# Kernel optimization log

Measured on AMD Instinct MI355X. Metric: run time of the kernel, lower is better.

## Reference

```python
import jax, jax.numpy as jnp
import numpy as np

N, E, D, H, C = 50000, 800000, 256, 8, 32  # C = D // H
STEPS = 6
NEG = 0.2  # leaky_relu negative slope (PyG HEATConv default)
ETD, EAD = 10, 50  # edge_type_emb_dim, edge_attr_emb_dim


def setup_inputs() -> dict:
    key = jax.random.key(0)
    ks = jax.random.split(key, 20)
    def g(k, shape, scale=0.05):
        return jax.random.normal(k, shape, dtype=jnp.float32) * scale
    return {
        "x": jax.random.normal(ks[0], (N, D), dtype=jnp.float32),
        "edge_index": jax.random.randint(ks[1], (2, E), 0, N),
        "edge_attr": jax.random.normal(ks[2], (E,), dtype=jnp.float32),
        "node_type": jax.random.randint(ks[3], (N,), 0, 2),
        "link_type": jax.random.randint(ks[4], (E,), 0, 3),
        # HEATConv params (shared across all 6 steps)
        "Wh": g(ks[5], (2, D, C)),          # HeteroLinear weight per node type
        "bh": g(ks[6], (2, C)),             # HeteroLinear bias per node type
        "Et": g(ks[7], (3, ETD)),           # edge type embedding table
        "Wea": g(ks[8], (1, EAD)),          # edge attr embedding (Linear, no bias)
        "Watt": g(ks[9], (2 * C + ETD + EAD, H)),  # attention (Linear, no bias)
        "Wlin": g(ks[10], (C + EAD, C)),    # message lin (Linear, no bias)
        # per-step FFN + LayerNorm params
        "ffn_w1": g(ks[11], (STEPS, D, 4 * D)),
        "ffn_b1": g(ks[12], (STEPS, 4 * D)),
        "ffn_w2": g(ks[13], (STEPS, 4 * D, D)),
        "ffn_b2": g(ks[14], (STEPS, D)),
        "ln1_g": jnp.ones((STEPS, D), jnp.float32),
        "ln1_b": jnp.zeros((STEPS, D), jnp.float32),
        "ln2_g": jnp.ones((STEPS, D), jnp.float32),
        "ln2_b": jnp.zeros((STEPS, D), jnp.float32),
    }


def _leaky(v):
    return jax.nn.leaky_relu(v, NEG)


def _layer_norm(h, g, b, eps=1e-5):
    mu = h.mean(-1, keepdims=True)
    var = h.var(-1, keepdims=True)  # biased, matches torch LayerNorm
    return (h - mu) * jax.lax.rsqrt(var + eps) * g + b


def _heat_conv(m, src, dst, edge_attr, node_type, link_type, Wh, bh, Et, Wea, Watt, Wlin):
    # node-type-specific linear (HeteroLinear, 2 types): compute both, select
    x_all = jnp.einsum('nd,tdc->tnc', m, Wh) + bh[:, None, :]     # [2,N,C]
    x = jnp.where(node_type[:, None] == 0, x_all[0], x_all[1])    # [N,C]
    ete = _leaky(Et[link_type])                                   # [E,ETD]
    eae = _leaky(edge_attr[:, None] @ Wea)                        # [E,EAD]
    feat = jnp.concatenate([x[dst], x[src], ete, eae], axis=-1)   # [E, 2C+ETD+EAD]
    logits = _leaky(feat @ Watt)                                  # [E,H]
    # segment softmax over incoming edges of each destination node
    mx = jax.ops.segment_max(logits, dst, num_segments=N)
    e = jnp.exp(logits - mx[dst])
    s = jax.ops.segment_sum(e, dst, num_segments=N)
    alpha = e / (s[dst] + 1e-16)                                  # [E,H]
    msg = jnp.concatenate([x[src], eae], axis=-1) @ Wlin          # [E,C]
    per_edge = alpha[:, :, None] * msg[:, None, :]                # [E,H,C]
    out = jax.ops.segment_sum(per_edge, dst, num_segments=N)      # [N,H,C]
    return out.reshape(N, H * C)  # concat heads; root_weight=False


def reference(x, edge_index, edge_attr, node_type, link_type, Wh, bh, Et, Wea, Watt, Wlin,
              ffn_w1, ffn_b1, ffn_w2, ffn_b2, ln1_g, ln1_b, ln2_g, ln2_b):
    src, dst = edge_index[0], edge_index[1]
    m = x
    for i in range(STEPS):
        h = _heat_conv(m, src, dst, edge_attr, node_type, link_type,
                       Wh, bh, Et, Wea, Watt, Wlin)
        m = _layer_norm(h + m, ln1_g[i], ln1_b[i])
        f = jax.nn.relu(m @ ffn_w1[i] + ffn_b1[i]) @ ffn_w2[i] + ffn_b2[i]
        m = _layer_norm(f + m, ln2_g[i], ln2_b[i])
    return m
```

## Files before the change

kernel.cpp:

```cpp
#include <hip/hip_runtime.h>

#define Nn 50000
#define Ee 800000
#define STEPSn 6
#define NP 49

typedef _Float16 half8 __attribute__((ext_vector_type(8)));
typedef _Float16 half4v __attribute__((ext_vector_type(4)));
typedef float floatx4 __attribute__((ext_vector_type(4)));

typedef __attribute__((address_space(1))) void gvoid_t;
typedef __attribute__((address_space(3))) void svoid_t;

__device__ __forceinline__ float leakyf(float v) { return v > 0.f ? v : 0.2f * v; }

__device__ __forceinline__ void gload16(const void* g, void* l) {
    __builtin_amdgcn_global_load_lds((const gvoid_t*)g, (svoid_t*)l, 16, 0, 0);
}

__global__ void k_count(const int* __restrict__ dst, int* __restrict__ cnt) {
    int e = blockIdx.x * 256 + threadIdx.x;
    if (e < Ee) atomicAdd(&cnt[dst[e]], 1);
}

__global__ __launch_bounds__(256) void k_scan1(const int* __restrict__ cnt,
                                               int* __restrict__ part) {
    int b = blockIdx.x, t = threadIdx.x;
    int s = 0;
#pragma unroll
    for (int j = 0; j < 4; ++j) {
        int idx = b * 1024 + j * 256 + t;
        if (idx < Nn) s += cnt[idx];
    }
#pragma unroll
    for (int d = 1; d < 64; d <<= 1) s += __shfl_xor(s, d);
    __shared__ int ws[4];
    if ((t & 63) == 0) ws[t >> 6] = s;
    __syncthreads();
    if (t == 0) part[b] = ws[0] + ws[1] + ws[2] + ws[3];
}

__global__ void k_scan2(const int* __restrict__ part, int* __restrict__ pref,
                        int* __restrict__ offN) {
    int t = threadIdx.x;
    int v = (t < NP) ? part[t] : 0;
    int p = v;
#pragma unroll
    for (int d = 1; d < 64; d <<= 1) {
        int u = __shfl_up(p, d);
        if (t >= d) p += u;
    }
    if (t < NP) pref[t] = p - v;
    if (t == 63) offN[0] = p;
}

__global__ __launch_bounds__(256) void k_scan3(const int* __restrict__ cnt,
                                               const int* __restrict__ pref,
                                               int* __restrict__ off) {
    __shared__ int wsum[4];
    int b = blockIdx.x, t = threadIdx.x;
    int base = b * 1024;
    int v[4];
    int s = 0;
#pragma unroll
    for (int j = 0; j < 4; ++j) {
        int idx = base + t * 4 + j;
        v[j] = (idx < Nn) ? cnt[idx] : 0;
        s += v[j];
    }
    int lane = t & 63, w = t >> 6;
    int ps = s;
#pragma unroll
    for (int d = 1; d < 64; d <<= 1) {
        int u = __shfl_up(ps, d);
        if (lane >= d) ps += u;
    }
    if (lane == 63) wsum[w] = ps;
    __syncthreads();
    int woff = 0;
    for (int i = 0; i < w; ++i) woff += wsum[i];
    int ex = pref[b] + woff + ps - s;
#pragma unroll
    for (int j = 0; j < 4; ++j) {
        int idx = base + t * 4 + j;
        if (idx < Nn) off[idx] = ex;
        ex += v[j];
    }
}

__global__ void k_fill(const int* __restrict__ src, const int* __restrict__ dst,
                       const float* __restrict__ edge_attr, const int* __restrict__ link_type,
                       const int* __restrict__ off, int* __restrict__ cur,
                       int2* __restrict__ edata) {
    int e = blockIdx.x * 256 + threadIdx.x;
    if (e >= Ee) return;
    int d = dst[e];
    int slot = off[d] + atomicAdd(&cur[d], 1);
    edata[slot] = make_int2(src[e] | (link_type[e] << 20), __float_as_int(edge_attr[e]));
}

__global__ void k_const(const float* __restrict__ Et, const float* __restrict__ Wea,
                        const float* __restrict__ Watt, const float* __restrict__ Wlin,
                        float* __restrict__ C) {
    __shared__ float u[50], v[50];
    int t = threadIdx.x;
    if (t < 50) {
        float w = Wea[t];
        u[t] = w * (w > 0.f ? 1.f : 0.2f);
        v[t] = w * (w < 0.f ? 1.f : 0.2f);
    }
    __syncthreads();
    if (t < 8) {
        float a = 0.f, b = 0.f;
        for (int j = 0; j < 50; ++j) {
            float w = Watt[(74 + j) * 8 + t];
            a += u[j] * w;
            b += v[j] * w;
        }
        C[t] = a;
        C[8 + t] = b;
    } else if (t < 32) {
        int lt = (t - 8) >> 3, h = (t - 8) & 7;
        float a = 0.f;
        for (int j = 0; j < 10; ++j) a += leakyf(Et[lt * 10 + j]) * Watt[(64 + j) * 8 + h];
        C[16 + (t - 8)] = a;
    } else if (t < 64) {
        int c = t - 32;
        float a = 0.f, b = 0.f;
        for (int j = 0; j < 50; ++j) {
            float w = Wlin[(32 + j) * 32 + c];
            a += u[j] * w;
            b += v[j] * w;
        }
        C[40 + c] = a;
        C[72 + c] = b;
    }
}

__global__ void k_comb(const float* __restrict__ Wh, const float* __restrict__ bh,
                       const float* __restrict__ Watt, const float* __restrict__ Wlin,
                       _Float16* __restrict__ Wcmb, float* __restrict__ bcmb) {
    int n = blockIdx.x;
    int k = threadIdx.x;
    if (n >= 96) {
        Wcmb[n * 256 + k] = (_Float16)0.f;
        return;
    }
    int ty = n / 48, c = n % 48;
    float a = 0.f;
    for (int kk = 0; kk < 32; ++kk) {
        float wsel;
        if (c < 32) wsel = Wlin[kk * 32 + c];
        else if (c < 40) wsel = Watt[kk * 8 + (c - 32)];
        else wsel = Watt[(32 + kk) * 8 + (c - 40)];
        a += Wh[ty * 8192 + k * 32 + kk] * wsel;
    }
    Wcmb[n * 256 + k] = (_Float16)a;
    if (k == 0) {
        float b = 0.f;
        for (int kk = 0; kk < 32; ++kk) {
            float wsel;
            if (c < 32) wsel = Wlin[kk * 32 + c];
            else if (c < 40) wsel = Watt[kk * 8 + (c - 32)];
            else wsel = Watt[(32 + kk) * 8 + (c - 40)];
            b += bh[ty * 32 + kk] * wsel;
        }
        bcmb[n] = b;
    }
}

__global__ void k_cvt(const float* __restrict__ x, _Float16* __restrict__ mh) {
    long i = ((long)blockIdx.x * 256 + threadIdx.x) * 4;
    if (i < (long)Nn * 256) {
        float4 v = *(const float4*)(x + i);
        half4v h;
        h[0] = (_Float16)v.x; h[1] = (_Float16)v.y;
        h[2] = (_Float16)v.z; h[3] = (_Float16)v.w;
        *(half4v*)(mh + i) = h;
    }
}

__global__ __launch_bounds__(256) void k_wtrans(const float* __restrict__ W,
                                                _Float16* __restrict__ WT,
                                                int K, int NN) {
    __shared__ float tile[64][65];
    int nk = K >> 6, nn = NN >> 6;
    int b = blockIdx.x;
    int s = b / (nk * nn);
    int r = b % (nk * nn);
    int kt = r / nn, nt = r % nn;
    const float* Ws = W + (long)s * K * NN;
    _Float16* WTs = WT + (long)s * K * NN;
    int lrow = threadIdx.x >> 6, lcol = threadIdx.x & 63;
#pragma unroll
    for (int i = 0; i < 16; ++i) {
        int row = i * 4 + lrow;
        tile[row][lcol] = Ws[(long)(kt * 64 + row) * NN + nt * 64 + lcol];
    }
    __syncthreads();
#pragma unroll
    for (int i = 0; i < 16; ++i) {
        int row = i * 4 + lrow;
        WTs[(long)(nt * 64 + row) * K + kt * 64 + lcol] = (_Float16)tile[lcol][row];
    }
}

__global__ __launch_bounds__(256) void k_node_proj2(
    const _Float16* __restrict__ mh, const int* __restrict__ node_type,
    const _Float16* __restrict__ Wcmb, const float* __restrict__ bcmb,
    float* __restrict__ adst, float* __restrict__ asrc,
    _Float16* __restrict__ xlin, int M) {
    __shared__ _Float16 sA[128 * 64];
    __shared__ _Float16 sB[128 * 64];
    __shared__ float sEpi[128][100];
    const int rowBase = blockIdx.x * 128;
    const int tid = threadIdx.x, wid = tid >> 6, lane = tid & 63;
    const int wm = (wid >> 1) * 64, wn = (wid & 1) * 64;

    floatx4 acc[4][4];
    floatx4 zz = {0.f, 0.f, 0.f, 0.f};
#pragma unroll
    for (int i = 0; i < 4; ++i)
#pragma unroll
        for (int j = 0; j < 4; ++j) acc[i][j] = zz;

    for (int k0 = 0; k0 < 256; k0 += 64) {
#pragma unroll
        for (int it = 0; it < 4; ++it) {
            int Ci = it * 256 + tid;
            int row = Ci >> 3, ch = Ci & 7;
            int gr = rowBase + row;
            if (gr > M - 1) gr = M - 1;
            gload16(mh + (long)gr * 256 + k0 + ((ch ^ (row & 7)) * 8),
                    &sA[(it * 256 + wid * 64) * 8]);
        }
#pragma unroll
        for (int it = 0; it < 4; ++it) {
            int Ci = it * 256 + tid;
            int row = Ci >> 3, ch = Ci & 7;
            gload16(Wcmb + (long)row * 256 + k0 + ((ch ^ (row & 7)) * 8),
                    &sB[(it * 256 + wid * 64) * 8]);
        }
        __syncthreads();
#pragma unroll
        for (int kk = 0; kk < 2; ++kk) {
            half8 af[4], bf[4];
#pragma unroll
            for (int i = 0; i < 4; ++i) {
                int row = wm + i * 16 + (lane & 15);
                int ch = (kk * 4 + (lane >> 4)) ^ (row & 7);
                af[i] = *(const half8*)&sA[row * 64 + ch * 8];
            }
#pragma unroll
            for (int j = 0; j < 4; ++j) {
                int row = wn + j * 16 + (lane & 15);
                int ch = (kk * 4 + (lane >> 4)) ^ (row & 7);
                bf[j] = *(const half8*)&sB[row * 64 + ch * 8];
            }
#pragma unroll
            for (int i = 0; i < 4; ++i)
#pragma unroll
                for (int j = 0; j < 4; ++j)
                    acc[i][j] = __builtin_amdgcn_mfma_f32_16x16x32_f16(af[i], bf[j], acc[i][j], 0, 0, 0);
        }
        __syncthreads();
    }
#pragma unroll
    for (int i = 0; i < 4; ++i)
#pragma unroll
        for (int j = 0; j < 4; ++j) {
            int col = wn + j * 16 + (lane & 15);
            if (col < 96) {
#pragma unroll
                for (int q = 0; q < 4; ++q)
                    sEpi[wm + i * 16 + (lane >> 4) * 4 + q][col] = acc[i][j][q];
            }
        }
    __syncthreads();
    for (int idx = tid; idx < 128 * 32; idx += 256) {
        int r = idx >> 5, c = idx & 31;
        int gr = rowBase + r;
        if (gr < M) {
            int ty = (node_type[gr] != 0) ? 1 : 0;
            int sc = ty * 48 + c;
            xlin[(long)gr * 32 + c] = (_Float16)(sEpi[r][sc] + bcmb[sc]);
        }
    }
    for (int idx = tid; idx < 128 * 8; idx += 256) {
        int r = idx >> 3, hh = idx & 7;
        int gr = rowBase + r;
        if (gr < M) {
            int ty = (node_type[gr] != 0) ? 1 : 0;
            adst[(long)gr * 8 + hh] = sEpi[r][ty * 48 + 32 + hh] + bcmb[ty * 48 + 32 + hh];
            asrc[(long)gr * 8 + hh] = sEpi[r][ty * 48 + 40 + hh] + bcmb[ty * 48 + 40 + hh];
        }
    }
}

__global__ __launch_bounds__(256) void k_edge_ln1(
    const int* __restrict__ off, const int2* __restrict__ edata,
    const float* __restrict__ C,
    const float* __restrict__ adst, const float* __restrict__ asrc,
    const _Float16* __restrict__ xlin, const float* __restrict__ m_in,
    const float* __restrict__ g1, const float* __restrict__ b1,
    _Float16* __restrict__ m1h) {
    __shared__ float sC[104];
    if (threadIdx.x < 104) sC[threadIdx.x] = C[threadIdx.x];
    __syncthreads();
    int n = blockIdx.x * 4 + (threadIdx.x >> 6);
    int lane = threadIdx.x & 63;
    long base = off[n];
    int deg = off[n + 1] - (int)base;
    int h = lane & 7;
    int hv = lane >> 5, lc = lane & 31;
    float adst_h = adst[(long)n * 8 + h];
    float linP = sC[40 + lc], linM = sC[72 + lc];
    float ssum = 0.f;
    float acc[8] = {0.f, 0.f, 0.f, 0.f, 0.f, 0.f, 0.f, 0.f};
    int deg2 = (deg + 1) & ~1;
    int i2 = hv;
    int2 edA = make_int2(0, 0);
    float asA = 0.f, xlA = 0.f;
    if (i2 < deg2) {
        long ei = base + (i2 < deg ? i2 : deg - 1);
        edA = edata[ei];
        int sA = edA.x & 0xFFFFF;
        asA = asrc[(long)sA * 8 + h];
        xlA = (float)xlin[(long)sA * 32 + lc];
    }
    while (i2 < deg2) {
        int i2n = i2 + 2;
        int2 edB = make_int2(0, 0);
        float asB = 0.f, xlB = 0.f;
        if (i2n < deg2) {
            long ein = base + (i2n < deg ? i2n : deg - 1);
            edB = edata[ein];
            int sB = edB.x & 0xFFFFF;
            asB = asrc[(long)sB * 8 + h];
            xlB = (float)xlin[(long)sB * 32 + lc];
        }
        bool valid = i2 < deg;
        int lt = edA.x >> 20;
        float t = __int_as_float(edA.y);
        float attc = sC[16 + lt * 8 + h] + t * (t > 0.f ? sC[h] : sC[8 + h]);
        float lg = adst_h + asA + attc;
        float w = valid ? __expf(leakyf(lg)) : 0.f;
        float msg = xlA + t * (t > 0.f ? linP : linM);
        if (lc < 8) ssum += w;
        int wbits = __float_as_int(w);
#define BCAST(HH)                                                                         \
        {                                                                                 \
            float whh = __int_as_float(__builtin_amdgcn_ds_swizzle(wbits, (HH) << 5));    \
            acc[HH] += whh * msg;                                                         \
        }
        BCAST(0) BCAST(1) BCAST(2) BCAST(3) BCAST(4) BCAST(5) BCAST(6) BCAST(7)
#undef BCAST
        edA = edB; asA = asB; xlA = xlB;
        i2 = i2n;
    }
#pragma unroll
    for (int hh = 0; hh < 8; ++hh) acc[hh] += __shfl_xor(acc[hh], 32);
    ssum += __shfl_xor(ssum, 32);
    float v[8];
    float s1 = 0.f, s2 = 0.f;
#pragma unroll
    for (int hh = 0; hh < 8; ++hh) {
        float sh = __shfl(ssum, hh);
        float o = acc[hh] / (sh + 1e-16f);
        float vv = o + m_in[(long)n * 256 + hh * 32 + lc];
        v[hh] = vv;
        s1 += vv;
        s2 += vv * vv;
    }
#pragma unroll
    for (int d = 1; d < 64; d <<= 1) { s1 += __shfl_xor(s1, d); s2 += __shfl_xor(s2, d); }
    float mu = s1 * (1.f / 512.f);
    float var = s2 * (1.f / 512.f) - mu * mu;
    float rs = rsqrtf(var + 1e-5f);
    if (hv == 0) {
#pragma unroll
        for (int hh = 0; hh < 8; ++hh) {
            int col = hh * 32 + lc;
            float o = (v[hh] - mu) * rs * g1[col] + b1[col];
            m1h[(long)n * 256 + col] = (_Float16)o;
        }
    }
}

__global__ __launch_bounds__(256) void k_ffn1(const _Float16* __restrict__ A,
                                              const _Float16* __restrict__ BT,
                                              const float* __restrict__ bias,
                                              _Float16* __restrict__ out,
                                              int M, int nRP) {
    __shared__ _Float16 sA[128 * 64];
    __shared__ _Float16 sB[128 * 64];
    __shared__ float sEpi[4][16][68];
    int bid = blockIdx.x;
    int xcd = bid & 7;
    int jj = bid >> 3;
    int ct = jj & 7;
    int rp = xcd + 8 * (jj >> 3);
    if (rp >= nRP) return;
    const int rowBase = rp * 128;
    const int colBase = ct * 128;
    const int tid = threadIdx.x, wid = tid >> 6, lane = tid & 63;
    const int wm = (wid >> 1) * 64, wn = (wid & 1) * 64;

    floatx4 acc[4][4];
    floatx4 zz = {0.f, 0.f, 0.f, 0.f};
#pragma unroll
    for (int i = 0; i < 4; ++i)
#pragma unroll
        for (int j = 0; j < 4; ++j) acc[i][j] = zz;

    for (int k0 = 0; k0 < 256; k0 += 64) {
#pragma unroll
        for (int it = 0; it < 4; ++it) {
            int Ci = it * 256 + tid;
            int row = Ci >> 3, ch = Ci & 7;
            int gr = rowBase + row;
            if (gr > M - 1) gr = M - 1;
            gload16(A + (long)gr * 256 + k0 + ((ch ^ (row & 7)) * 8),
                    &sA[(it * 256 + wid * 64) * 8]);
        }
#pragma unroll
        for (int it = 0; it < 4; ++it) {
            int Ci = it * 256 + tid;
            int row = Ci >> 3, ch = Ci & 7;
            gload16(BT + (long)(colBase + row) * 256 + k0 + ((ch ^ (row & 7)) * 8),
                    &sB[(it * 256 + wid * 64) * 8]);
        }
        __syncthreads();
#pragma unroll
        for (int kk = 0; kk < 2; ++kk) {
            half8 af[4], bf[4];
#pragma unroll
            for (int i = 0; i < 4; ++i) {
                int row = wm + i * 16 + (lane & 15);
                int ch = (kk * 4 + (lane >> 4)) ^ (row & 7);
                af[i] = *(const half8*)&sA[row * 64 + ch * 8];
            }
#pragma unroll
            for (int j = 0; j < 4; ++j) {
                int row = wn + j * 16 + (lane & 15);
                int ch = (kk * 4 + (lane >> 4)) ^ (row & 7);
                bf[j] = *(const half8*)&sB[row * 64 + ch * 8];
            }
#pragma unroll
            for (int i = 0; i < 4; ++i)
#pragma unroll
                for (int j = 0; j < 4; ++j)
                    acc[i][j] = __builtin_amdgcn_mfma_f32_16x16x32_f16(af[i], bf[j], acc[i][j], 0, 0, 0);
        }
        __syncthreads();
    }
#pragma unroll
    for (int i = 0; i < 4; ++i) {
#pragma unroll
        for (int j = 0; j < 4; ++j)
#pragma unroll
            for (int q = 0; q < 4; ++q)
                sEpi[wid][(lane >> 4) * 4 + q][j * 16 + (lane & 15)] = acc[i][j][q];
        __asm__ volatile("s_waitcnt lgkmcnt(0)");
#pragma unroll
        for (int it = 0; it < 4; ++it) {
            int r16 = it * 4 + (lane >> 4);
            float4 vv = *(const float4*)&sEpi[wid][r16][(lane & 15) * 4];
            int grow = rowBase + wm + i * 16 + r16;
            int gcol = colBase + wn + (lane & 15) * 4;
            if (grow < M) {
                float4 bv = *(const float4*)&bias[gcol];
                float o0 = vv.x + bv.x, o1 = vv.y + bv.y, o2 = vv.z + bv.z, o3 = vv.w + bv.w;
                o0 = o0 > 0.f ? o0 : 0.f;
                o1 = o1 > 0.f ? o1 : 0.f;
                o2 = o2 > 0.f ? o2 : 0.f;
                o3 = o3 > 0.f ? o3 : 0.f;
                half4v hv;
                hv[0] = (_Float16)o0; hv[1] = (_Float16)o1;
                hv[2] = (_Float16)o2; hv[3] = (_Float16)o3;
                *(half4v*)&out[(long)grow * 1024 + gcol] = hv;
            }
        }
        __asm__ volatile("s_waitcnt lgkmcnt(0)");
    }
}

__global__ __launch_bounds__(512) void k_ffn2(const _Float16* __restrict__ A,
                                              const _Float16* __restrict__ BT,
                                              const float* __restrict__ bias,
                                              const _Float16* __restrict__ resid,
                                              const float* __restrict__ g2,
                                              const float* __restrict__ b2,
                                              float* __restrict__ outp,
                                              _Float16* __restrict__ outh, int M) {
    __shared__ _Float16 sA[128 * 64];
    __shared__ _Float16 sB[256 * 64];
    __shared__ float sS1[2][128], sS2[2][128];
    const int rowBase = blockIdx.x * 128;
    const int tid = threadIdx.x, wid = tid >> 6, lane = tid & 63;
    const int wm = (wid >> 1) * 32, wn = (wid & 1) * 128, cg = wid & 1;

    floatx4 acc[2][8];
    floatx4 zz = {0.f, 0.f, 0.f, 0.f};
#pragma unroll
    for (int i = 0; i < 2; ++i)
#pragma unroll
        for (int j = 0; j < 8; ++j) acc[i][j] = zz;

    for (int k0 = 0; k0 < 1024; k0 += 64) {
#pragma unroll
        for (int it = 0; it < 2; ++it) {
            int Ci = it * 512 + tid;
            int row = Ci >> 3, ch = Ci & 7;
            int gr = rowBase + row;
            if (gr > M - 1) gr = M - 1;
            gload16(A + (long)gr * 1024 + k0 + ((ch ^ (row & 7)) * 8),
                    &sA[(it * 512 + wid * 64) * 8]);
        }
#pragma unroll
        for (int it = 0; it < 4; ++it) {
            int Ci = it * 512 + tid;
            int row = Ci >> 3, ch = Ci & 7;
            gload16(BT + (long)row * 1024 + k0 + ((ch ^ (row & 7)) * 8),
                    &sB[(it * 512 + wid * 64) * 8]);
        }
        __syncthreads();
#pragma unroll
        for (int kk = 0; kk < 2; ++kk) {
            half8 af[2], bf[8];
#pragma unroll
            for (int i = 0; i < 2; ++i) {
                int row = wm + i * 16 + (lane & 15);
                int ch = (kk * 4 + (lane >> 4)) ^ (row & 7);
                af[i] = *(const half8*)&sA[row * 64 + ch * 8];
            }
#pragma unroll
            for (int j = 0; j < 8; ++j) {
                int row = wn + j * 16 + (lane & 15);
                int ch = (kk * 4 + (lane >> 4)) ^ (row & 7);
                bf[j] = *(const half8*)&sB[row * 64 + ch * 8];
            }
#pragma unroll
            for (int i = 0; i < 2; ++i)
#pragma unroll
                for (int j = 0; j < 8; ++j)
                    acc[i][j] = __builtin_amdgcn_mfma_f32_16x16x32_f16(af[i], bf[j], acc[i][j], 0, 0, 0);
        }
        __syncthreads();
    }
#pragma unroll
    for (int i = 0; i < 2; ++i) {
#pragma unroll
        for (int q = 0; q < 4; ++q) {
            int rl = wm + i * 16 + (lane >> 4) * 4 + q;
            long grow = rowBase + rl;
            long gr = grow > M - 1 ? M - 1 : grow;
            float s1 = 0.f, s2 = 0.f;
#pragma unroll
            for (int j = 0; j < 8; ++j) {
                int gcol = wn + j * 16 + (lane & 15);
                float v = acc[i][j][q] + bias[gcol] + (float)resid[gr * 256 + gcol];
                acc[i][j][q] = v;
                s1 += v;
                s2 += v * v;
            }
#pragma unroll
            for (int d = 1; d < 16; d <<= 1) {
                s1 += __shfl_xor(s1, d);
                s2 += __shfl_xor(s2, d);
            }
            if ((lane & 15) == 0) {
                sS1[cg][rl] = s1;
                sS2[cg][rl] = s2;
            }
        }
    }
    __syncthreads();
#pragma unroll
    for (int i = 0; i < 2; ++i) {
#pragma unroll
        for (int q = 0; q < 4; ++q) {
            int rl = wm + i * 16 + (lane >> 4) * 4 + q;
            long grow = rowBase + rl;
            if (grow < M) {
                float t1 = sS1[0][rl] + sS1[1][rl];
                float t2 = sS2[0][rl] + sS2[1][rl];
                float mu = t1 * (1.f / 256.f);
                float var = t2 * (1.f / 256.f) - mu * mu;
                float rs = rsqrtf(var + 1e-5f);
#pragma unroll
                for (int j = 0; j < 8; ++j) {
                    int gcol = wn + j * 16 + (lane & 15);
                    float o = (acc[i][j][q] - mu) * rs * g2[gcol] + b2[gcol];
                    outp[grow * 256 + gcol] = o;
                    outh[grow * 256 + gcol] = (_Float16)o;
                }
            }
        }
    }
}

__global__ void k_fail(float* out) {
    if (threadIdx.x == 0 && blockIdx.x == 0) out[0] = 2.0e6f;
}

extern "C" void kernel_launch(void* const* d_in, const int* in_sizes, int n_in,
                              void* d_out, int out_size, void* d_ws, size_t ws_size,
                              hipStream_t stream) {
    const float* x = (const float*)d_in[0];
    const int* ei = (const int*)d_in[1];
    const float* edge_attr = (const float*)d_in[2];
    const int* node_type = (const int*)d_in[3];
    const int* link_type = (const int*)d_in[4];
    const float* Wh = (const float*)d_in[5];
    const float* bh = (const float*)d_in[6];
    const float* Et = (const float*)d_in[7];
    const float* Wea = (const float*)d_in[8];
    const float* Watt = (const float*)d_in[9];
    const float* Wlin = (const float*)d_in[10];
    const float* ffn_w1 = (const float*)d_in[11];
    const float* ffn_b1 = (const float*)d_in[12];
    const float* ffn_w2 = (const float*)d_in[13];
    const float* ffn_b2 = (const float*)d_in[14];
    const float* ln1_g = (const float*)d_in[15];
    const float* ln1_b = (const float*)d_in[16];
    const float* ln2_g = (const float*)d_in[17];
    const float* ln2_b = (const float*)d_in[18];
    const int* srcp = ei;
    const int* dstp = ei + Ee;

    size_t o = 0;
    auto carve = [&](size_t bytes) -> void* {
        void* p = (char*)d_ws + o;
        o += (bytes + 255) & ~(size_t)255;
        return p;
    };
    _Float16* m1h = (_Float16*)carve((size_t)Nn * 256 * 2);
    _Float16* mh = (_Float16*)carve((size_t)Nn * 256 * 2);
    float* adst = (float*)carve((size_t)Nn * 8 * 4);
    float* asrc = (float*)carve((size_t)Nn * 8 * 4);
    _Float16* xlin = (_Float16*)carve((size_t)Nn * 32 * 2);
    int2* edata = (int2*)carve((size_t)Ee * 8);
    int* off = (int*)carve((size_t)(Nn + 1) * 4);
    int* cnt = (int*)carve((size_t)Nn * 4);
    int* cur = (int*)carve((size_t)Nn * 4);
    int* part = (int*)carve(64 * 4);
    int* pref = (int*)carve(64 * 4);
    _Float16* W1T = (_Float16*)carve((size_t)STEPSn * 256 * 1024 * 2);
    _Float16* W2T = (_Float16*)carve((size_t)STEPSn * 256 * 1024 * 2);
    _Float16* Wcmb = (_Float16*)carve(128 * 256 * 2);
    float* bcmb = (float*)carve(128 * 4);
    float* econst = (float*)carve(104 * 4);
    long remain = (long)ws_size - (long)o;
    long ch = remain / 2048;
    ch = (ch / 128) * 128;
    int CH = ch > Nn ? Nn : (int)ch;
    if (CH < 128) {
        k_fail<<<1, 64, 0, stream>>>((float*)d_out);
        return;
    }
    _Float16* f1h = (_Float16*)carve((size_t)CH * 1024 * 2);
    if (o > ws_size) {
        k_fail<<<1, 64, 0, stream>>>((float*)d_out);
        return;
    }

    hipMemsetAsync(cnt, 0, (size_t)Nn * 4, stream);
    hipMemsetAsync(cur, 0, (size_t)Nn * 4, stream);
    k_count<<<3125, 256, 0, stream>>>(dstp, cnt);
    k_scan1<<<NP, 256, 0, stream>>>(cnt, part);
    k_scan2<<<1, 64, 0, stream>>>(part, pref, off + Nn);
    k_scan3<<<NP, 256, 0, stream>>>(cnt, pref, off);
    k_fill<<<3125, 256, 0, stream>>>(srcp, dstp, edge_attr, link_type, off, cur, edata);
    k_const<<<1, 128, 0, stream>>>(Et, Wea, Watt, Wlin, econst);
    k_comb<<<128, 256, 0, stream>>>(Wh, bh, Watt, Wlin, Wcmb, bcmb);
    k_cvt<<<12500, 256, 0, stream>>>(x, mh);
    k_wtrans<<<STEPSn * 64, 256, 0, stream>>>(ffn_w1, W1T, 256, 1024);
    k_wtrans<<<STEPSn * 64, 256, 0, stream>>>(ffn_w2, W2T, 1024, 256);

    const float* m_in = x;
    for (int s = 0; s < STEPSn; ++s) {
        k_node_proj2<<<(Nn + 127) / 128, 256, 0, stream>>>(mh, node_type, Wcmb, bcmb,
                                                           adst, asrc, xlin, Nn);
        k_edge_ln1<<<Nn / 4, 256, 0, stream>>>(off, edata, econst, adst, asrc,
                                               xlin, m_in, ln1_g + s * 256, ln1_b + s * 256,
                                               m1h);
        for (int cs = 0; cs < Nn; cs += CH) {
            int cm = (Nn - cs) < CH ? (Nn - cs) : CH;
            int nRP = (cm + 127) / 128;
            int nRPpad = ((nRP + 7) / 8) * 8;
            k_ffn1<<<nRPpad * 8, 256, 0, stream>>>(
                m1h + (size_t)cs * 256, W1T + (size_t)s * 262144,
                ffn_b1 + s * 1024, f1h, cm, nRP);
            k_ffn2<<<nRP, 512, 0, stream>>>(
                f1h, W2T + (size_t)s * 262144, ffn_b2 + s * 256,
                m1h + (size_t)cs * 256, ln2_g + s * 256, ln2_b + s * 256,
                (float*)d_out + (size_t)cs * 256, mh + (size_t)cs * 256, cm);
        }
        m_in = (const float*)d_out;
    }
}
```

Before: 1.296 ms.

## Fuse FFN1 and FFN2 into one kernel keeping hidden activations on chip

Merges the two FFN GEMM kernels into a single k_ffn that computes each 128-column chunk of the hidden layer into shared memory and immediately accumulates it into the second GEMM, then applies LayerNorm. This removes the global round-trip of the 50000x1024 fp16 intermediate. The fp32 output is written only on the last step, and the edge kernel now reads an fp16 residual instead of fp32. It also replaces the ds_swizzle head broadcasts with DPP quad-perm broadcasts plus a final swap. Trade-offs are lower occupancy from the large shared-memory footprint and launch bounds, only about 391 blocks, and slight precision loss from the fp16 residual.

Measured after the change: 1.395 ms. 1.08x slower.

```diff
diff --git a/kernel.cpp b/kernel.cpp
--- a/kernel.cpp
+++ b/kernel.cpp
@@ -16,6 +16,12 @@
 
 __device__ __forceinline__ void gload16(const void* g, void* l) {
     __builtin_amdgcn_global_load_lds((const gvoid_t*)g, (svoid_t*)l, 16, 0, 0);
+}
+
+template <int CTRL>
+__device__ __forceinline__ float dppf(float v) {
+    return __int_as_float(__builtin_amdgcn_update_dpp(
+        0, __float_as_int(v), CTRL, 0xF, 0xF, true));
 }
 
 __global__ void k_count(const int* __restrict__ dst, int* __restrict__ cnt) {
@@ -301,7 +307,7 @@
     const int* __restrict__ off, const int2* __restrict__ edata,
     const float* __restrict__ C,
     const float* __restrict__ adst, const float* __restrict__ asrc,
-    const _Float16* __restrict__ xlin, const float* __restrict__ m_in,
+    const _Float16* __restrict__ xlin, const _Float16* __restrict__ mres,
     const float* __restrict__ g1, const float* __restrict__ b1,
     _Float16* __restrict__ m1h) {
     __shared__ float sC[104];
@@ -347,16 +353,26 @@
         float w = valid ? __expf(leakyf(lg)) : 0.f;
         float msg = xlA + t * (t > 0.f ? linP : linM);
         if (lc < 8) ssum += w;
-        int wbits = __float_as_int(w);
-#define BCAST(HH)                                                                         \
-        {                                                                                 \
-            float whh = __int_as_float(__builtin_amdgcn_ds_swizzle(wbits, (HH) << 5));    \
-            acc[HH] += whh * msg;                                                         \
-        }
-        BCAST(0) BCAST(1) BCAST(2) BCAST(3) BCAST(4) BCAST(5) BCAST(6) BCAST(7)
-#undef BCAST
+        float w4 = dppf<0x124>(w);
+        acc[0] += dppf<0x00>(w) * msg;
+        acc[1] += dppf<0x55>(w) * msg;
+        acc[2] += dppf<0xAA>(w) * msg;
+        acc[3] += dppf<0xFF>(w) * msg;
+        acc[4] += dppf<0x00>(w4) * msg;
+        acc[5] += dppf<0x55>(w4) * msg;
+        acc[6] += dppf<0xAA>(w4) * msg;
+        acc[7] += dppf<0xFF>(w4) * msg;
         edA = edB; asA = asB; xlA = xlB;
         i2 = i2n;
+    }
+    {
+        bool sw = (lane & 4) != 0;
+#pragma unroll
+        for (int k = 0; k < 4; ++k) {
+            float a = acc[k], b = acc[4 + k];
+            acc[k] = sw ? b : a;
+            acc[4 + k] = sw ? a : b;
+        }
     }
 #pragma unroll
     for (int hh = 0; hh < 8; ++hh) acc[hh] += __shfl_xor(acc[hh], 32);
@@ -367,7 +383,7 @@
     for (int hh = 0; hh < 8; ++hh) {
         float sh = __shfl(ssum, hh);
         float o = acc[hh] / (sh + 1e-16f);
-        float vv = o + m_in[(long)n * 256 + hh * 32 + lc];
+        float vv = o + (float)mres[(long)n * 256 + hh * 32 + lc];
         v[hh] = vv;
         s1 += vv;
         s2 += vv * vv;
@@ -387,182 +403,141 @@
     }
 }
 
-__global__ __launch_bounds__(256) void k_ffn1(const _Float16* __restrict__ A,
-                                              const _Float16* __restrict__ BT,
-                                              const float* __restrict__ bias,
-                                              _Float16* __restrict__ out,
-                                              int M, int nRP) {
-    __shared__ _Float16 sA[128 * 64];
-    __shared__ _Float16 sB[128 * 64];
-    __shared__ float sEpi[4][16][68];
-    int bid = blockIdx.x;
-    int xcd = bid & 7;
-    int jj = bid >> 3;
-    int ct = jj & 7;
-    int rp = xcd + 8 * (jj >> 3);
-    if (rp >= nRP) return;
-    const int rowBase = rp * 128;
-    const int colBase = ct * 128;
+#define HP 136
+__global__ __launch_bounds__(512, 2) void k_ffn(
+    const _Float16* __restrict__ A, const _Float16* __restrict__ W1,
+    const float* __restrict__ b1, const _Float16* __restrict__ W2,
+    const float* __restrict__ b2, const float* __restrict__ g2,
+    const float* __restrict__ bln2, float* __restrict__ outp,
+    _Float16* __restrict__ outh, int M, int writeOut) {
+    __shared__ _Float16 sA[128 * 256];
+    __shared__ _Float16 sH[128 * HP];
+    __shared__ _Float16 sW[256 * 64];
+    __shared__ float sS1[4][128], sS2[4][128];
     const int tid = threadIdx.x, wid = tid >> 6, lane = tid & 63;
-    const int wm = (wid >> 1) * 64, wn = (wid & 1) * 64;
-
-    floatx4 acc[4][4];
+    const int rowBase = blockIdx.x * 128;
+    const int wtm = (wid >> 2) * 64;
+    const int wtn1 = (wid & 3) * 32;
+    const int wtn2 = (wid & 3) * 64;
+
+#pragma unroll
+    for (int it = 0; it < 8; ++it) {
+        int Ci = it * 512 + tid;
+        int row = Ci >> 5, c = Ci & 31;
+        int gr = rowBase + row;
+        if (gr > M - 1) gr = M - 1;
+        int cs = (c & 24) | ((c & 7) ^ (row & 7));
+        gload16(A + (long)gr * 256 + cs * 8, &sA[(it * 512 + wid * 64) * 8]);
+    }
+
+    floatx4 acc2[4][4];
     floatx4 zz = {0.f, 0.f, 0.f, 0.f};
 #pragma unroll
     for (int i = 0; i < 4; ++i)
 #pragma unroll
-        for (int j = 0; j < 4; ++j) acc[i][j] = zz;
-
-    for (int k0 = 0; k0 < 256; k0 += 64) {
-#pragma unroll
-        for (int it = 0; it < 4; ++it) {
-            int Ci = it * 256 + tid;
-            int row = Ci >> 3, ch = Ci & 7;
-            int gr = rowBase + row;
-            if (gr > M - 1) gr = M - 1;
-            gload16(A + (long)gr * 256 + k0 + ((ch ^ (row & 7)) * 8),
-                    &sA[(it * 256 + wid * 64) * 8]);
-        }
-#pragma unroll
-        for (int it = 0; it < 4; ++it) {
-            int Ci = it * 256 + tid;
-            int row = Ci >> 3, ch = Ci & 7;
-            gload16(BT + (long)(colBase + row) * 256 + k0 + ((ch ^ (row & 7)) * 8),
-                    &sB[(it * 256 + wid * 64) * 8]);
-        }
-        __syncthreads();
-#pragma unroll
-        for (int kk = 0; kk < 2; ++kk) {
-            half8 af[4], bf[4];
-#pragma unroll
-            for (int i = 0; i < 4; ++i) {
-                int row = wm + i * 16 + (lane & 15);
-                int ch = (kk * 4 + (lane >> 4)) ^ (row & 7);
-                af[i] = *(const half8*)&sA[row * 64 + ch * 8];
-            }
+        for (int j = 0; j < 4; ++j) acc2[i][j] = zz;
+
+    for (int ct = 0; ct < 8; ++ct) {
+        floatx4 acc1[4][2];
+#pragma unroll
+        for (int i = 0; i < 4; ++i)
+#pragma unroll
+            for (int j = 0; j < 2; ++j) acc1[i][j] = zz;
+        for (int ks = 0; ks < 4; ++ks) {
+#pragma unroll
+            for (int it = 0; it < 2; ++it) {
+                int Ci = it * 512 + tid;
+                int row = Ci >> 3, ch = Ci & 7;
+                gload16(W1 + (long)(ct * 128 + row) * 256 + ks * 64 + ((ch ^ (row & 7)) * 8),
+                        &sW[(it * 512 + wid * 64) * 8]);
+            }
+            __syncthreads();
+#pragma unroll
+            for (int kk = 0; kk < 2; ++kk) {
+                half8 af[4], bf[2];
+#pragma unroll
+                for (int i = 0; i < 4; ++i) {
+                    int row = wtm + i * 16 + (lane & 15);
+                    int c = ks * 8 + kk * 4 + (lane >> 4);
+                    int cs = (c & 24) | ((c & 7) ^ (row & 7));
+                    af[i] = *(const half8*)&sA[row * 256 + cs * 8];
+                }
+#pragma unroll
+                for (int j = 0; j < 2; ++j) {
+                    int row = wtn1 + j * 16 + (lane & 15);
+                    int ch = (kk * 4 + (lane >> 4)) ^ (row & 7);
+                    bf[j] = *(const half8*)&sW[(row * 8 + ch) * 8];
+                }
+#pragma unroll
+                for (int i = 0; i < 4; ++i)
+#pragma unroll
+                    for (int j = 0; j < 2; ++j)
+                        acc1[i][j] = __builtin_amdgcn_mfma_f32_16x16x32_f16(af[i], bf[j], acc1[i][j], 0, 0, 0);
+            }
+            __syncthreads();
+        }
+#pragma unroll
+        for (int j = 0; j < 2; ++j) {
+            int kl = wtn1 + j * 16 + (lane & 15);
+            float bv = b1[ct * 128 + kl];
+#pragma unroll
+            for (int i = 0; i < 4; ++i)
+#pragma unroll
+                for (int q = 0; q < 4; ++q) {
+                    int m = wtm + i * 16 + (lane >> 4) * 4 + q;
+                    float vv = acc1[i][j][q] + bv;
+                    sH[m * HP + kl] = (_Float16)(vv > 0.f ? vv : 0.f);
+                }
+        }
+        for (int ks2 = 0; ks2 < 2; ++ks2) {
+#pragma unroll
+            for (int it = 0; it < 4; ++it) {
+                int Ci = it * 512 + tid;
+                int row = Ci >> 3, ch = Ci & 7;
+                gload16(W2 + (long)row * 1024 + ct * 128 + ks2 * 64 + ((ch ^ (row & 7)) * 8),
+                        &sW[(it * 512 + wid * 64) * 8]);
+            }
+            __syncthreads();
+#pragma unroll
+            for (int kk = 0; kk < 2; ++kk) {
+                half8 af[4], bf[4];
+#pragma unroll
+                for (int i = 0; i < 4; ++i) {
+                    int m = wtm + i * 16 + (lane & 15);
+                    af[i] = *(const half8*)&sH[m * HP + ks2 * 64 + (kk * 4 + (lane >> 4)) * 8];
+                }
+#pragma unroll
+                for (int j = 0; j < 4; ++j) {
+                    int nc = wtn2 + j * 16 + (lane & 15);
+                    int ch = (kk * 4 + (lane >> 4)) ^ (nc & 7);
+                    bf[j] = *(const half8*)&sW[(nc * 8 + ch) * 8];
+                }
+#pragma unroll
+                for (int i = 0; i < 4; ++i)
+#pragma unroll
+                    for (int j = 0; j < 4; ++j)
+                        acc2[i][j] = __builtin_amdgcn_mfma_f32_16x16x32_f16(af[i], bf[j], acc2[i][j], 0, 0, 0);
+            }
+            __syncthreads();
+        }
+    }
+    const int cg = wid & 3;
+#pragma unroll
+    for (int i = 0; i < 4; ++i) {
+#pragma unroll
+        for (int q = 0; q < 4; ++q) {
+            int rl = wtm + i * 16 + (lane >> 4) * 4 + q;
+            float s1 = 0.f, s2 = 0.f;
 #pragma unroll
             for (int j = 0; j < 4; ++j) {
-                int row = wn + j * 16 + (lane & 15);
-                int ch = (kk * 4 + (lane >> 4)) ^ (row & 7);
-                bf[j] = *(const half8*)&sB[row * 64 + ch * 8];
-            }
-#pragma unroll
-            for (int i = 0; i < 4; ++i)
-#pragma unroll
-                for (int j = 0; j < 4; ++j)
-                    acc[i][j] = __builtin_amdgcn_mfma_f32_16x16x32_f16(af[i], bf[j], acc[i][j], 0, 0, 0);
-        }
-        __syncthreads();
-    }
-#pragma unroll
-    for (int i = 0; i < 4; ++i) {
-#pragma unroll
-        for (int j = 0; j < 4; ++j)
-#pragma unroll
-            for (int q = 0; q < 4; ++q)
-                sEpi[wid][(lane >> 4) * 4 + q][j * 16 + (lane & 15)] = acc[i][j][q];
-        __asm__ volatile("s_waitcnt lgkmcnt(0)");
-#pragma unroll
-        for (int it = 0; it < 4; ++it) {
-            int r16 = it * 4 + (lane >> 4);
-            float4 vv = *(const float4*)&sEpi[wid][r16][(lane & 15) * 4];
-            int grow = rowBase + wm + i * 16 + r16;
-            int gcol = colBase + wn + (lane & 15) * 4;
-            if (grow < M) {
-                float4 bv = *(const float4*)&bias[gcol];
-                float o0 = vv.x + bv.x, o1 = vv.y + bv.y, o2 = vv.z + bv.z, o3 = vv.w + bv.w;
-                o0 = o0 > 0.f ? o0 : 0.f;
-                o1 = o1 > 0.f ? o1 : 0.f;
-                o2 = o2 > 0.f ? o2 : 0.f;
-                o3 = o3 > 0.f ? o3 : 0.f;
-                half4v hv;
-                hv[0] = (_Float16)o0; hv[1] = (_Float16)o1;
-                hv[2] = (_Float16)o2; hv[3] = (_Float16)o3;
-                *(half4v*)&out[(long)grow * 1024 + gcol] = hv;
-            }
-        }
-        __asm__ volatile("s_waitcnt lgkmcnt(0)");
-    }
-}
-
-__global__ __launch_bounds__(512) void k_ffn2(const _Float16* __restrict__ A,
-                                              const _Float16* __restrict__ BT,
-                                              const float* __restrict__ bias,
-                                              const _Float16* __restrict__ resid,
-                                              const float* __restrict__ g2,
-                                              const float* __restrict__ b2,
-                                              float* __restrict__ outp,
-                                              _Float16* __restrict__ outh, int M) {
-    __shared__ _Float16 sA[128 * 64];
-    __shared__ _Float16 sB[256 * 64];
-    __shared__ float sS1[2][128], sS2[2][128];
-    const int rowBase = blockIdx.x * 128;
-    const int tid = threadIdx.x, wid = tid >> 6, lane = tid & 63;
-    const int wm = (wid >> 1) * 32, wn = (wid & 1) * 128, cg = wid & 1;
-
-    floatx4 acc[2][8];
-    floatx4 zz = {0.f, 0.f, 0.f, 0.f};
-#pragma unroll
-    for (int i = 0; i < 2; ++i)
-#pragma unroll
-        for (int j = 0; j < 8; ++j) acc[i][j] = zz;
-
-    for (int k0 = 0; k0 < 1024; k0 += 64) {
-#pragma unroll
-        for (int it = 0; it < 2; ++it) {
-            int Ci = it * 512 + tid;
-            int row = Ci >> 3, ch = Ci & 7;
-            int gr = rowBase + row;
-            if (gr > M - 1) gr = M - 1;
-            gload16(A + (long)gr * 1024 + k0 + ((ch ^ (row & 7)) * 8),
-                    &sA[(it * 512 + wid * 64) * 8]);
-        }
-#pragma unroll
-        for (int it = 0; it < 4; ++it) {
-            int Ci = it * 512 + tid;
-            int row = Ci >> 3, ch = Ci & 7;
-            gload16(BT + (long)row * 1024 + k0 + ((ch ^ (row & 7)) * 8),
-                    &sB[(it * 512 + wid * 64) * 8]);
-        }
-        __syncthreads();
-#pragma unroll
-        for (int kk = 0; kk < 2; ++kk) {
-            half8 af[2], bf[8];
-#pragma unroll
-            for (int i = 0; i < 2; ++i) {
-                int row = wm + i * 16 + (lane & 15);
-                int ch = (kk * 4 + (lane >> 4)) ^ (row & 7);
-                af[i] = *(const half8*)&sA[row * 64 + ch * 8];
-            }
-#pragma unroll
-            for (int j = 0; j < 8; ++j) {
-                int row = wn + j * 16 + (lane & 15);
-                int ch = (kk * 4 + (lane >> 4)) ^ (row & 7);
-                bf[j] = *(const half8*)&sB[row * 64 + ch * 8];
-            }
-#pragma unroll
-            for (int i = 0; i < 2; ++i)
-#pragma unroll
-                for (int j = 0; j < 8; ++j)
-                    acc[i][j] = __builtin_amdgcn_mfma_f32_16x16x32_f16(af[i], bf[j], acc[i][j], 0, 0, 0);
-        }
-        __syncthreads();
-    }
-#pragma unroll
-    for (int i = 0; i < 2; ++i) {
-#pragma unroll
-        for (int q = 0; q < 4; ++q) {
-            int rl = wm + i * 16 + (lane >> 4) * 4 + q;
-            long grow = rowBase + rl;
-            long gr = grow > M - 1 ? M - 1 : grow;
-            float s1 = 0.f, s2 = 0.f;
-#pragma unroll
-            for (int j = 0; j < 8; ++j) {
-                int gcol = wn + j * 16 + (lane & 15);
-                float v = acc[i][j][q] + bias[gcol] + (float)resid[gr * 256 + gcol];
-                acc[i][j][q] = v;
-                s1 += v;
-                s2 += v * v;
+                int col = wtn2 + j * 16 + (lane & 15);
+                int cs = col >> 3;
+                int csw = (cs & 24) | ((cs & 7) ^ (rl & 7));
+                float rv = (float)sA[rl * 256 + csw * 8 + (col & 7)];
+                float vv = acc2[i][j][q] + b2[col] + rv;
+                acc2[i][j][q] = vv;
+                s1 += vv;
+                s2 += vv * vv;
             }
 #pragma unroll
             for (int d = 1; d < 16; d <<= 1) {
@@ -577,23 +552,23 @@
     }
     __syncthreads();
 #pragma unroll
-    for (int i = 0; i < 2; ++i) {
+    for (int i = 0; i < 4; ++i) {
 #pragma unroll
         for (int q = 0; q < 4; ++q) {
-            int rl = wm + i * 16 + (lane >> 4) * 4 + q;
+            int rl = wtm + i * 16 + (lane >> 4) * 4 + q;
             long grow = rowBase + rl;
             if (grow < M) {
-                float t1 = sS1[0][rl] + sS1[1][rl];
-                float t2 = sS2[0][rl] + sS2[1][rl];
+                float t1 = sS1[0][rl] + sS1[1][rl] + sS1[2][rl] + sS1[3][rl];
+                float t2 = sS2[0][rl] + sS2[1][rl] + sS2[2][rl] + sS2[3][rl];
                 float mu = t1 * (1.f / 256.f);
                 float var = t2 * (1.f / 256.f) - mu * mu;
                 float rs = rsqrtf(var + 1e-5f);
 #pragma unroll
-                for (int j = 0; j < 8; ++j) {
-                    int gcol = wn + j * 16 + (lane & 15);
-                    float o = (acc[i][j][q] - mu) * rs * g2[gcol] + b2[gcol];
-                    outp[grow * 256 + gcol] = o;
-                    outh[grow * 256 + gcol] = (_Float16)o;
+                for (int j = 0; j < 4; ++j) {
+                    int col = wtn2 + j * 16 + (lane & 15);
+                    float o = (acc2[i][j][q] - mu) * rs * g2[col] + bln2[col];
+                    outh[grow * 256 + col] = (_Float16)o;
+                    if (writeOut) outp[grow * 256 + col] = o;
                 }
             }
         }
@@ -651,15 +626,6 @@
     _Float16* Wcmb = (_Float16*)carve(128 * 256 * 2);
     float* bcmb = (float*)carve(128 * 4);
     float* econst = (float*)carve(104 * 4);
-    long remain = (long)ws_size - (long)o;
-    long ch = remain / 2048;
-    ch = (ch / 128) * 128;
-    int CH = ch > Nn ? Nn : (int)ch;
-    if (CH < 128) {
-        k_fail<<<1, 64, 0, stream>>>((float*)d_out);
-        return;
-    }
-    _Float16* f1h = (_Float16*)carve((size_t)CH * 1024 * 2);
     if (o > ws_size) {
         k_fail<<<1, 64, 0, stream>>>((float*)d_out);
         return;
@@ -678,25 +644,17 @@
     k_wtrans<<<STEPSn * 64, 256, 0, stream>>>(ffn_w1, W1T, 256, 1024);
     k_wtrans<<<STEPSn * 64, 256, 0, stream>>>(ffn_w2, W2T, 1024, 256);
 
-    const float* m_in = x;
+    const int nRP = (Nn + 127) / 128;
     for (int s = 0; s < STEPSn; ++s) {
-        k_node_proj2<<<(Nn + 127) / 128, 256, 0, stream>>>(mh, node_type, Wcmb, bcmb,
-                                                           adst, asrc, xlin, Nn);
+        k_node_proj2<<<nRP, 256, 0, stream>>>(mh, node_type, Wcmb, bcmb,
+                                              adst, asrc, xlin, Nn);
         k_edge_ln1<<<Nn / 4, 256, 0, stream>>>(off, edata, econst, adst, asrc,
-                                               xlin, m_in, ln1_g + s * 256, ln1_b + s * 256,
+                                               xlin, mh, ln1_g + s * 256, ln1_b + s * 256,
                                                m1h);
-        for (int cs = 0; cs < Nn; cs += CH) {
-            int cm = (Nn - cs) < CH ? (Nn - cs) : CH;
-            int nRP = (cm + 127) / 128;
-            int nRPpad = ((nRP + 7) / 8) * 8;
-            k_ffn1<<<nRPpad * 8, 256, 0, stream>>>(
-                m1h + (size_t)cs * 256, W1T + (size_t)s * 262144,
-                ffn_b1 + s * 1024, f1h, cm, nRP);
-            k_ffn2<<<nRP, 512, 0, stream>>>(
-                f1h, W2T + (size_t)s * 262144, ffn_b2 + s * 256,
-                m1h + (size_t)cs * 256, ln2_g + s * 256, ln2_b + s * 256,
-                (float*)d_out + (size_t)cs * 256, mh + (size_t)cs * 256, cm);
-        }
-        m_in = (const float*)d_out;
-    }
-}
+        k_ffn<<<nRP, 512, 0, stream>>>(m1h, W1T + (size_t)s * 262144,
+                                       ffn_b1 + s * 1024, W2T + (size_t)s * 262144,
+                                       ffn_b2 + s * 256, ln2_g + s * 256, ln2_b + s * 256,
+                                       (float*)d_out, mh, Nn,
+                                       (s == STEPSn - 1) ? 1 : 0);
+    }
+}
```

## Use fp16 residual, write fp32 output only on last step, DPP head broadcast

Applied to the files above, without the earlier changes.

The edge/LN1 kernel now reads the residual from the fp16 copy of m instead of the fp32 output buffer, so the FFN2 kernel writes the fp32 output only on the final step. This cuts fp32 traffic per step. The edge loop is unrolled to process two edge pairs per iteration with deeper prefetch, and the per-head weight broadcast uses DPP quad permutes instead of ds_swizzle, followed by a lane-dependent swap to fix head order. The fp16 residual lowers precision of the residual add in steps after the first, including step 0 where x is now rounded to fp16.

Measured after the change: 1.233 ms. -4.9%, faster.

```diff
diff --git a/kernel.cpp b/kernel.cpp
--- a/kernel.cpp
+++ b/kernel.cpp
@@ -16,6 +16,12 @@
 
 __device__ __forceinline__ void gload16(const void* g, void* l) {
     __builtin_amdgcn_global_load_lds((const gvoid_t*)g, (svoid_t*)l, 16, 0, 0);
+}
+
+template <int CTRL>
+__device__ __forceinline__ float dppf(float v) {
+    return __int_as_float(__builtin_amdgcn_update_dpp(
+        0, __float_as_int(v), CTRL, 0xF, 0xF, true));
 }
 
 __global__ void k_count(const int* __restrict__ dst, int* __restrict__ cnt) {
@@ -301,7 +307,7 @@
     const int* __restrict__ off, const int2* __restrict__ edata,
     const float* __restrict__ C,
     const float* __restrict__ adst, const float* __restrict__ asrc,
-    const _Float16* __restrict__ xlin, const float* __restrict__ m_in,
+    const _Float16* __restrict__ xlin, const _Float16* __restrict__ mres,
     const float* __restrict__ g1, const float* __restrict__ b1,
     _Float16* __restrict__ m1h) {
     __shared__ float sC[104];
@@ -317,46 +323,67 @@
     float linP = sC[40 + lc], linM = sC[72 + lc];
     float ssum = 0.f;
     float acc[8] = {0.f, 0.f, 0.f, 0.f, 0.f, 0.f, 0.f, 0.f};
-    int deg2 = (deg + 1) & ~1;
-    int i2 = hv;
-    int2 edA = make_int2(0, 0);
-    float asA = 0.f, xlA = 0.f;
-    if (i2 < deg2) {
-        long ei = base + (i2 < deg ? i2 : deg - 1);
-        edA = edata[ei];
-        int sA = edA.x & 0xFFFFF;
-        asA = asrc[(long)sA * 8 + h];
-        xlA = (float)xlin[(long)sA * 32 + lc];
-    }
-    while (i2 < deg2) {
-        int i2n = i2 + 2;
-        int2 edB = make_int2(0, 0);
-        float asB = 0.f, xlB = 0.f;
-        if (i2n < deg2) {
-            long ein = base + (i2n < deg ? i2n : deg - 1);
-            edB = edata[ein];
-            int sB = edB.x & 0xFFFFF;
-            asB = asrc[(long)sB * 8 + h];
-            xlB = (float)xlin[(long)sB * 32 + lc];
-        }
-        bool valid = i2 < deg;
-        int lt = edA.x >> 20;
-        float t = __int_as_float(edA.y);
-        float attc = sC[16 + lt * 8 + h] + t * (t > 0.f ? sC[h] : sC[8 + h]);
-        float lg = adst_h + asA + attc;
-        float w = valid ? __expf(leakyf(lg)) : 0.f;
-        float msg = xlA + t * (t > 0.f ? linP : linM);
-        if (lc < 8) ssum += w;
-        int wbits = __float_as_int(w);
-#define BCAST(HH)                                                                         \
-        {                                                                                 \
-            float whh = __int_as_float(__builtin_amdgcn_ds_swizzle(wbits, (HH) << 5));    \
-            acc[HH] += whh * msg;                                                         \
-        }
-        BCAST(0) BCAST(1) BCAST(2) BCAST(3) BCAST(4) BCAST(5) BCAST(6) BCAST(7)
-#undef BCAST
-        edA = edB; asA = asB; xlA = xlB;
-        i2 = i2n;
+
+#define ELOAD(IDX, ED, AS, XL)                                  \
+    {                                                           \
+        int ci_ = (IDX) < deg ? (IDX) : deg - 1;                \
+        long ei_ = base + ci_;                                  \
+        ED = edata[ei_];                                        \
+        int s_ = ED.x & 0xFFFFF;                                \
+        AS = asrc[(long)s_ * 8 + h];                            \
+        XL = (float)xlin[(long)s_ * 32 + lc];                   \
+    }
+#define ECOMP(IDX, ED, AS, XL)                                                         \
+    {                                                                                  \
+        bool valid_ = (IDX) < deg;                                                     \
+        int lt_ = ED.x >> 20;                                                          \
+        float t_ = __int_as_float(ED.y);                                               \
+        float attc_ = sC[16 + lt_ * 8 + h] + t_ * (t_ > 0.f ? sC[h] : sC[8 + h]);      \
+        float lg_ = adst_h + AS + attc_;                                               \
+        float w_ = valid_ ? __expf(leakyf(lg_)) : 0.f;                                 \
+        float msg_ = XL + t_ * (t_ > 0.f ? linP : linM);                               \
+        if (lc < 8) ssum += w_;                                                        \
+        float w4_ = dppf<0x124>(w_);                                                   \
+        acc[0] += dppf<0x00>(w_) * msg_;                                               \
+        acc[1] += dppf<0x55>(w_) * msg_;                                               \
+        acc[2] += dppf<0xAA>(w_) * msg_;                                               \
+        acc[3] += dppf<0xFF>(w_) * msg_;                                               \
+        acc[4] += dppf<0x00>(w4_) * msg_;                                              \
+        acc[5] += dppf<0x55>(w4_) * msg_;                                              \
+        acc[6] += dppf<0xAA>(w4_) * msg_;                                              \
+        acc[7] += dppf<0xFF>(w4_) * msg_;                                              \
+    }
+
+    if (deg > 0) {
+        int deg4 = (deg + 3) & ~3;
+        int i = hv;
+        int2 e0, e1;
+        float a0, x0, a1, x1;
+        ELOAD(i, e0, a0, x0);
+        ELOAD(i + 2, e1, a1, x1);
+        for (; i < deg4; i += 4) {
+            int2 f0 = make_int2(0, 0), f1 = make_int2(0, 0);
+            float b0 = 0.f, y0 = 0.f, b1v = 0.f, y1 = 0.f;
+            if (i + 4 < deg4) {
+                ELOAD(i + 4, f0, b0, y0);
+                ELOAD(i + 6, f1, b1v, y1);
+            }
+            ECOMP(i, e0, a0, x0);
+            ECOMP(i + 2, e1, a1, x1);
+            e0 = f0; a0 = b0; x0 = y0;
+            e1 = f1; a1 = b1v; x1 = y1;
+        }
+    }
+#undef ELOAD
+#undef ECOMP
+    {
+        bool sw = (lane & 4) != 0;
+#pragma unroll
+        for (int k = 0; k < 4; ++k) {
+            float a = acc[k], b = acc[4 + k];
+            acc[k] = sw ? b : a;
+            acc[4 + k] = sw ? a : b;
+        }
     }
 #pragma unroll
     for (int hh = 0; hh < 8; ++hh) acc[hh] += __shfl_xor(acc[hh], 32);
@@ -367,7 +394,7 @@
     for (int hh = 0; hh < 8; ++hh) {
         float sh = __shfl(ssum, hh);
         float o = acc[hh] / (sh + 1e-16f);
-        float vv = o + m_in[(long)n * 256 + hh * 32 + lc];
+        float vv = o + (float)mres[(long)n * 256 + hh * 32 + lc];
         v[hh] = vv;
         s1 += vv;
         s2 += vv * vv;
@@ -492,7 +519,8 @@
                                               const float* __restrict__ g2,
                                               const float* __restrict__ b2,
                                               float* __restrict__ outp,
-                                              _Float16* __restrict__ outh, int M) {
+                                              _Float16* __restrict__ outh,
+                                              int M, int writeOut) {
     __shared__ _Float16 sA[128 * 64];
     __shared__ _Float16 sB[256 * 64];
     __shared__ float sS1[2][128], sS2[2][128];
@@ -592,8 +620,8 @@
                 for (int j = 0; j < 8; ++j) {
                     int gcol = wn + j * 16 + (lane & 15);
                     float o = (acc[i][j][q] - mu) * rs * g2[gcol] + b2[gcol];
-                    outp[grow * 256 + gcol] = o;
                     outh[grow * 256 + gcol] = (_Float16)o;
+                    if (writeOut) outp[grow * 256 + gcol] = o;
                 }
             }
         }
@@ -678,13 +706,13 @@
     k_wtrans<<<STEPSn * 64, 256, 0, stream>>>(ffn_w1, W1T, 256, 1024);
     k_wtrans<<<STEPSn * 64, 256, 0, stream>>>(ffn_w2, W2T, 1024, 256);
 
-    const float* m_in = x;
     for (int s = 0; s < STEPSn; ++s) {
         k_node_proj2<<<(Nn + 127) / 128, 256, 0, stream>>>(mh, node_type, Wcmb, bcmb,
                                                            adst, asrc, xlin, Nn);
         k_edge_ln1<<<Nn / 4, 256, 0, stream>>>(off, edata, econst, adst, asrc,
-                                               xlin, m_in, ln1_g + s * 256, ln1_b + s * 256,
+                                               xlin, mh, ln1_g + s * 256, ln1_b + s * 256,
                                                m1h);
+        int writeOut = (s == STEPSn - 1) ? 1 : 0;
         for (int cs = 0; cs < Nn; cs += CH) {
             int cm = (Nn - cs) < CH ? (Nn - cs) : CH;
             int nRP = (cm + 127) / 128;
@@ -695,8 +723,7 @@
             k_ffn2<<<nRP, 512, 0, stream>>>(
                 f1h, W2T + (size_t)s * 262144, ffn_b2 + s * 256,
                 m1h + (size_t)cs * 256, ln2_g + s * 256, ln2_b + s * 256,
-                (float*)d_out + (size_t)cs * 256, mh + (size_t)cs * 256, cm);
-        }
-        m_in = (const float*)d_out;
-    }
-}
+                (float*)d_out + (size_t)cs * 256, mh + (size_t)cs * 256, cm, writeOut);
+        }
+    }
+}
```
